# Optimization experiments

Hardware: AMD Instinct MI355X
Metric: run time of the kernel (lower is better)

Reference implementation:

```python
import jax, jax.numpy as jnp
import numpy as np

H = 2048      # hidden_dim
NH = 32       # num_heads
HD = H // NH  # head_dim


def setup_inputs() -> dict:
    key = jax.random.key(0)
    ks = jax.random.split(key, 9)
    s = 1.0 / np.sqrt(H)
    return {
        "hidden_states": jax.random.normal(ks[0], (2, 2048, H), dtype=jnp.float32),
        "wq": jax.random.uniform(ks[1], (H, H), jnp.float32, -s, s),
        "bq": jnp.zeros((H,), jnp.float32),
        "wk": jax.random.uniform(ks[2], (H, H), jnp.float32, -s, s),
        "bk": jnp.zeros((H,), jnp.float32),
        "wv": jax.random.uniform(ks[3], (H, H), jnp.float32, -s, s),
        "bv": jnp.zeros((H,), jnp.float32),
        "wo": jax.random.uniform(ks[4], (H, H), jnp.float32, -s, s),
        "bo": jnp.zeros((H,), jnp.float32),
    }


def reference(hidden_states, wq, bq, wk, bk, wv, bv, wo, bo):
    B, S, _ = hidden_states.shape
    def heads(x):  # [B,S,H] -> [B,NH,S,HD]
        return x.reshape(B, S, NH, HD).transpose(0, 2, 1, 3)
    q = heads(hidden_states @ wq.T + bq)
    k = heads(hidden_states @ wk.T + bk)
    v = heads(hidden_states @ wv.T + bv)
    scores = jnp.einsum("bhqd,bhkd->bhqk", q, k) / np.sqrt(HD).astype(np.float32)
    causal = jnp.tril(jnp.ones((S, S), dtype=bool))
    scores = jnp.where(causal, scores, -jnp.inf)
    attn = jax.nn.softmax(scores, axis=-1)
    out = jnp.einsum("bhqk,bhkd->bhqd", attn, v)
    out = out.transpose(0, 2, 1, 3).reshape(B, S, H)
    return out @ wo.T + bo
```

## Files before the change

### kernel.cpp

```cpp
#include <hip/hip_runtime.h>
#include <hip/hip_bf16.h>

#define HDIM 2048
#define NHEADS 32
#define HEADD 64
#define NBATCH 2
#define SEQLEN 2048
#define MTOT (NBATCH * SEQLEN)
#define NQT (SEQLEN / 128)
#define LDQKV 6144

typedef __bf16 bf16;
typedef __bf16 bf16x8 __attribute__((ext_vector_type(8)));
typedef float f32x4 __attribute__((ext_vector_type(4)));
typedef float f32x8 __attribute__((ext_vector_type(8)));
typedef float f32x16 __attribute__((ext_vector_type(16)));

__device__ __forceinline__ void gload_lds16(const bf16* g, bf16* l) {
  __builtin_amdgcn_global_load_lds(
      (const __attribute__((address_space(1))) void*)g,
      (__attribute__((address_space(3))) void*)l, 16, 0, 0);
}

__device__ __forceinline__ unsigned cvtpk_bf16(float lo, float hi) {
  unsigned r;
  asm("v_cvt_pk_bf16_f32 %0, %1, %2" : "=v"(r) : "v"(lo), "v"(hi));
  return r;
}

__device__ __forceinline__ float max3f(float a, float b, float c) {
  float r;
  asm("v_max3_f32 %0, %1, %2, %3" : "=v"(r) : "v"(a), "v"(b), "v"(c));
  return r;
}

__global__ void __launch_bounds__(256) cvt_f32_to_bf16(
    const float* __restrict__ src, bf16* __restrict__ dst, int n) {
  int i = (blockIdx.x * 256 + threadIdx.x) * 8;
  if (i >= n) return;
  f32x8 a = *(const f32x8*)(src + i);
  bf16x8 o;
#pragma unroll
  for (int j = 0; j < 8; ++j) o[j] = (bf16)a[j];
  *(bf16x8*)(dst + i) = o;
}

__global__ void __launch_bounds__(256) cvt4_f32_to_bf16(
    const float* __restrict__ s0, const float* __restrict__ s1,
    const float* __restrict__ s2, const float* __restrict__ s3,
    bf16* __restrict__ d0, bf16* __restrict__ d1,
    bf16* __restrict__ d2, bf16* __restrict__ d3) {
  const float* src; bf16* dst;
  switch (blockIdx.y) {
    case 0: src = s0; dst = d0; break;
    case 1: src = s1; dst = d1; break;
    case 2: src = s2; dst = d2; break;
    default: src = s3; dst = d3; break;
  }
  int i = (blockIdx.x * 256 + threadIdx.x) * 8;
  f32x8 a = *(const f32x8*)(src + i);
  bf16x8 o;
#pragma unroll
  for (int j = 0; j < 8; ++j) o[j] = (bf16)a[j];
  *(bf16x8*)(dst + i) = o;
}

__global__ void __launch_bounds__(256) pack_bias(
    const float* __restrict__ bq, const float* __restrict__ bk,
    const float* __restrict__ bv, float* __restrict__ out) {
  int i = blockIdx.x * 256 + threadIdx.x;
  if (i >= LDQKV) return;
  float v;
  if (i < HDIM) v = bq[i];
  else if (i < 2 * HDIM) v = bk[i - HDIM];
  else v = bv[i - 2 * HDIM];
  out[i] = v;
}

template <bool OUT_F32>
__global__ void __launch_bounds__(256, 2) gemmq(
    const bf16* __restrict__ A, const bf16* __restrict__ W,
    const float* __restrict__ bias, void* __restrict__ Cout,
    int Ndim, float scale) {
  constexpr int NT = 64;
  __shared__ bf16 As[2][256 * 32];
  __shared__ bf16 Bs[3][192 * 32];

  const int tid = threadIdx.x;
  const int l = tid & 63;
  const int w = tid >> 6;
  const int wm = w >> 1;
  const int wn = w & 1;

  const int wid = blockIdx.x;
  const int j = wid >> 3;
  const int m0 = ((wid & 7) * 2 + (j & 1)) * 256;
  const int n0 = (j >> 1) * 192;

  const int rowA = tid >> 2;
  const int cg = (((tid & 3) ^ ((tid >> 3) & 3))) * 8;

  auto stgA = [&](int s, int kt) {
    const bf16* g = A + (size_t)m0 * 2048 + kt * 32 + cg;
#pragma unroll
    for (int i = 0; i < 4; ++i)
      gload_lds16(g + (size_t)(i * 64 + rowA) * 2048,
                  &As[s][(i * 256 + w * 64) * 8]);
  };
  auto stgB = [&](int s, int kt) {
    const bf16* g = W + (size_t)n0 * 2048 + kt * 32 + cg;
#pragma unroll
    for (int i = 0; i < 3; ++i)
      gload_lds16(g + (size_t)(i * 64 + rowA) * 2048,
                  &Bs[s][(i * 256 + w * 64) * 8]);
  };

  f32x4 acc[8][6];
#pragma unroll
  for (int mf = 0; mf < 8; ++mf)
#pragma unroll
    for (int nf = 0; nf < 6; ++nf) acc[mf][nf] = {0.f, 0.f, 0.f, 0.f};

  const int fr = l & 15;
  const int fch = (((l >> 4) ^ ((fr >> 1) & 3))) * 8;
  const int abase = (wm * 128 + fr) * 32 + fch;
  const int bbase = (wn * 96 + fr) * 32 + fch;

  stgA(0, 0);
  stgB(0, 0);
  stgB(1, 1);
  asm volatile("s_waitcnt vmcnt(3)" ::: "memory");
  __builtin_amdgcn_s_barrier();

  int sb = 0;
  for (int t = 0; t < NT; ++t) {
    const int sa = t & 1;
    int sb2 = sb + 2; if (sb2 >= 3) sb2 -= 3;

    bf16x8 bf[6], af[4];
#pragma unroll
    for (int nf = 0; nf < 6; ++nf)
      bf[nf] = *(const bf16x8*)&Bs[sb][bbase + nf * 16 * 32];
#pragma unroll
    for (int f = 0; f < 4; ++f)
      af[f] = *(const bf16x8*)&As[sa][abase + f * 16 * 32];

    if (t + 1 < NT) stgA(sa ^ 1, t + 1);
    if (t + 2 < NT) stgB(sb2, t + 2);

    __builtin_amdgcn_s_setprio(1);
#pragma unroll
    for (int f = 0; f < 4; ++f)
#pragma unroll
      for (int nf = 0; nf < 6; ++nf)
        acc[f][nf] = __builtin_amdgcn_mfma_f32_16x16x32_bf16(
            af[f], bf[nf], acc[f][nf], 0, 0, 0);
    __builtin_amdgcn_s_setprio(0);

#pragma unroll
    for (int f = 0; f < 4; ++f)
      af[f] = *(const bf16x8*)&As[sa][abase + (4 + f) * 16 * 32];

    __builtin_amdgcn_s_setprio(1);
#pragma unroll
    for (int f = 0; f < 4; ++f)
#pragma unroll
      for (int nf = 0; nf < 6; ++nf)
        acc[4 + f][nf] = __builtin_amdgcn_mfma_f32_16x16x32_bf16(
            af[f], bf[nf], acc[4 + f][nf], 0, 0, 0);
    __builtin_amdgcn_s_setprio(0);

    if (t < NT - 2)
      asm volatile("s_waitcnt vmcnt(3)" ::: "memory");
    else
      asm volatile("s_waitcnt vmcnt(0)" ::: "memory");
    __builtin_amdgcn_s_barrier();

    sb = (sb == 2) ? 0 : sb + 1;
  }

  const int rj = (l >> 4) * 4;
#pragma unroll
  for (int mf = 0; mf < 8; ++mf)
#pragma unroll
    for (int nf = 0; nf < 6; ++nf) {
      const int col = n0 + wn * 96 + nf * 16 + fr;
      const float secsc = (col < 2048) ? scale : 1.0f;
      const float bvl = bias[col];
#pragma unroll
      for (int jj = 0; jj < 4; ++jj) {
        const int row = m0 + wm * 128 + mf * 16 + rj + jj;
        const float v = (acc[mf][nf][jj] + bvl) * secsc;
        if constexpr (OUT_F32)
          ((float*)Cout)[(size_t)row * Ndim + col] = v;
        else
          ((bf16*)Cout)[(size_t)row * Ndim + col] = (bf16)v;
      }
    }
}

template <int BM, bool OUT_F32>
__global__ void __launch_bounds__(512, 2) gemm3(
    const bf16* __restrict__ A, const bf16* __restrict__ W,
    const float* __restrict__ bias, void* __restrict__ Cout,
    int Ndim, float scale) {
  constexpr int NT = 64;
  constexpr int FM = BM / 32;
  constexpr int ALD = BM / 128;
  constexpr int LPT = ALD + 2;
  constexpr int MPX = (4096 / BM) / 8;
  __shared__ bf16 As[4][BM * 32];
  __shared__ bf16 Bs[4][256 * 32];

  const int tid = threadIdx.x;
  const int l = tid & 63;
  const int w = tid >> 6;
  const int wm = w >> 2;
  const int wn = w & 3;

  const int wid = blockIdx.x;
  const int j = wid >> 3;
  const int m0 = ((wid & 7) * MPX + (j & (MPX - 1))) * BM;
  const int n0 = (j / MPX) * 256;

  const float secsc = (n0 < 2048) ? scale : 1.0f;

  const int rowA = tid >> 2;
  const int cg = (((tid & 3) ^ ((tid >> 3) & 3))) * 8;

  auto stageA = [&](int s, int kt) {
    const int k0 = kt * 32 + cg;
#pragma unroll
    for (int i = 0; i < ALD; ++i)
      gload_lds16(A + (size_t)(m0 + i * 128 + rowA) * 2048 + k0,
                  &As[s][(i * 512 + w * 64) * 8]);
  };
  auto stageB = [&](int s, int kt) {
    const int k0 = kt * 32 + cg;
#pragma unroll
    for (int i = 0; i < 2; ++i)
      gload_lds16(W + (size_t)(n0 + i * 128 + rowA) * 2048 + k0,
                  &Bs[s][(i * 512 + w * 64) * 8]);
  };

  f32x4 acc[FM][4];
#pragma unroll
  for (int mf = 0; mf < FM; ++mf)
#pragma unroll
    for (int nf = 0; nf < 4; ++nf) acc[mf][nf] = {0.f, 0.f, 0.f, 0.f};

  const int fr = l & 15;
  const int fch = (((l >> 4) ^ ((fr >> 1) & 3))) * 8;

  stageA(0, 0); stageB(0, 0);
  stageA(1, 1); stageB(1, 1);
  stageA(2, 2); stageB(2, 2);
  if constexpr (LPT == 4)
    asm volatile("s_waitcnt vmcnt(8)" ::: "memory");
  else
    asm volatile("s_waitcnt vmcnt(6)" ::: "memory");
  __builtin_amdgcn_s_barrier();

  for (int t = 0; t < NT; ++t) {
    const int s = t & 3;
    const int sn = (t + 3) & 3;
    const bool st = (t + 3) < NT;

    bf16x8 bf[4], af[FM];
#pragma unroll
    for (int nf = 0; nf < 4; ++nf)
      bf[nf] = *(const bf16x8*)&Bs[s][(wn * 64 + nf * 16 + fr) * 32 + fch];
#pragma unroll
    for (int f = 0; f < FM; ++f)
      af[f] = *(const bf16x8*)&As[s][(wm * (BM / 2) + f * 16 + fr) * 32 + fch];

    if (st) { stageA(sn, t + 3); stageB(sn, t + 3); }

    __builtin_amdgcn_s_setprio(1);
#pragma unroll
    for (int f = 0; f < FM; ++f)
#pragma unroll
      for (int nf = 0; nf < 4; ++nf)
        acc[f][nf] = __builtin_amdgcn_mfma_f32_16x16x32_bf16(
            af[f], bf[nf], acc[f][nf], 0, 0, 0);
    __builtin_amdgcn_s_setprio(0);

    if (t < NT - 3) {
      if constexpr (LPT == 4)
        asm volatile("s_waitcnt vmcnt(8)" ::: "memory");
      else
        asm volatile("s_waitcnt vmcnt(6)" ::: "memory");
    } else if (t == NT - 3) {
      if constexpr (LPT == 4)
        asm volatile("s_waitcnt vmcnt(4)" ::: "memory");
      else
        asm volatile("s_waitcnt vmcnt(3)" ::: "memory");
    } else if (t == NT - 2) {
      asm volatile("s_waitcnt vmcnt(0)" ::: "memory");
    }
    if (t < NT - 1) __builtin_amdgcn_s_barrier();
  }

  const int rj = (l >> 4) * 4;
#pragma unroll
  for (int mf = 0; mf < FM; ++mf)
#pragma unroll
    for (int nf = 0; nf < 4; ++nf) {
      const int col = n0 + wn * 64 + nf * 16 + fr;
      const float bvl = bias[col];
#pragma unroll
      for (int jj = 0; jj < 4; ++jj) {
        const int row = m0 + wm * (BM / 2) + mf * 16 + rj + jj;
        const float v = (acc[mf][nf][jj] + bvl) * secsc;
        if constexpr (OUT_F32)
          ((float*)Cout)[(size_t)row * Ndim + col] = v;
        else
          ((bf16*)Cout)[(size_t)row * Ndim + col] = (bf16)v;
      }
    }
}

__global__ void __launch_bounds__(256) transpose_v(
    const bf16* __restrict__ QKV, bf16* __restrict__ Vt) {
  __shared__ bf16 T[64][72];
  const int t = threadIdx.x;
  const int s0 = blockIdx.x * 64;
  const int h = blockIdx.y, b = blockIdx.z;
  const size_t inb = (size_t)b * SEQLEN * LDQKV + 2 * HDIM + (size_t)h * HEADD;
#pragma unroll
  for (int i = 0; i < 2; ++i) {
    const int idx = t + i * 256;
    const int r = idx >> 3, c = (idx & 7) * 8;
    *(bf16x8*)&T[r][c] = *(const bf16x8*)&QKV[inb + (size_t)(s0 + r) * LDQKV + c];
  }
  __syncthreads();
  const size_t outb = (size_t)(b * NHEADS + h) * HEADD * SEQLEN + s0;
#pragma unroll
  for (int i = 0; i < 2; ++i) {
    const int idx = t + i * 256;
    const int d = idx >> 3, cs = (idx & 7) * 8;
    bf16x8 o;
#pragma unroll
    for (int j = 0; j < 8; ++j) o[j] = T[cs + j][d];
    *(bf16x8*)&Vt[outb + (size_t)d * SEQLEN + cs] = o;
  }
}

__global__ void __launch_bounds__(256) attn4(
    const bf16* __restrict__ QKV, const bf16* __restrict__ Vt,
    bf16* __restrict__ O) {
  __shared__ bf16 Kl[2][64 * 64];
  __shared__ bf16 Vl[2][64 * 64];

  const int tid = threadIdx.x;
  const int l = tid & 63;
  const int w = tid >> 6;
  const int lq = l & 31;
  const int g = l >> 5;
  const int h = blockIdx.y, b = blockIdx.z;
  const size_t baseQ = (size_t)b * SEQLEN * LDQKV + (size_t)h * HEADD;
  const size_t baseK = baseQ + HDIM;
  const size_t baseV = (size_t)(b * NHEADS + h) * HEADD * SEQLEN;
  const size_t baseO = (size_t)b * SEQLEN * HDIM + (size_t)h * HEADD;

  const int L0 = w * 128 + l;
  const int L1 = w * 128 + 64 + l;
  const int r0 = L0 >> 3, gc0 = ((L0 & 7) ^ (r0 & 7)) * 8;
  const int r1 = L1 >> 3, gc1 = ((L1 & 7) ^ (r1 & 7)) * 8;
  const int dst0 = (w * 128) * 8;
  const int dst1 = (w * 128 + 64) * 8;

  auto stage = [&](int bufi, int kt) {
    const int k0s = kt * 64;
    gload_lds16(QKV + baseK + (size_t)(k0s + r0) * LDQKV + gc0, &Kl[bufi][dst0]);
    gload_lds16(QKV + baseK + (size_t)(k0s + r1) * LDQKV + gc1, &Kl[bufi][dst1]);
    gload_lds16(Vt + baseV + (size_t)r0 * SEQLEN + k0s + gc0, &Vl[bufi][dst0]);
    gload_lds16(Vt + baseV + (size_t)r1 * SEQLEN + k0s + gc1, &Vl[bufi][dst1]);
  };

#pragma unroll
  for (int seg = 0; seg < 2; ++seg) {
    const int qt = seg ? blockIdx.x : (NQT - 1 - blockIdx.x);
    const int q0 = qt * 128;
    const int qw = q0 + w * 32;
    const int qa = qw + lq;

    bf16x8 qf[4];
#pragma unroll
    for (int ks = 0; ks < 4; ++ks)
      qf[ks] = *(const bf16x8*)&QKV[baseQ + (size_t)qa * LDQKV + ks * 16 + g * 8];

    f32x16 oacc0, oacc1;
#pragma unroll
    for (int r = 0; r < 16; ++r) { oacc0[r] = 0.f; oacc1[r] = 0.f; }
    float mrun = -__builtin_inff(), lrun = 0.f;

    const int nkt = q0 / 64 + 2;
    stage(0, 0);

    for (int kt = 0; kt < nkt; ++kt) {
      const int cur = kt & 1;
      const int k0 = kt * 64;
      if (kt + 1 < nkt) {
        stage(cur ^ 1, kt + 1);
        asm volatile("s_waitcnt vmcnt(4)" ::: "memory");
      } else {
        asm volatile("s_waitcnt vmcnt(0)" ::: "memory");
      }
      __builtin_amdgcn_s_barrier();

      if (k0 <= qw + 31) {
        f32x16 st0, st1;
#pragma unroll
        for (int r = 0; r < 16; ++r) { st0[r] = 0.f; st1[r] = 0.f; }
        __builtin_amdgcn_s_setprio(1);
#pragma unroll
        for (int ks = 0; ks < 4; ++ks) {
          const int cr = (((2 * ks + g) ^ (lq & 7))) * 8;
          bf16x8 kf0 = *(const bf16x8*)&Kl[cur][lq * 64 + cr];
          bf16x8 kf1 = *(const bf16x8*)&Kl[cur][(32 + lq) * 64 + cr];
          st0 = __builtin_amdgcn_mfma_f32_32x32x16_bf16(kf0, qf[ks], st0, 0, 0, 0);
          st1 = __builtin_amdgcn_mfma_f32_32x32x16_bf16(kf1, qf[ks], st1, 0, 0, 0);
        }
        __builtin_amdgcn_s_setprio(0);

        if (k0 + 63 > qw) {
#pragma unroll
          for (int r = 0; r < 16; ++r) {
            const int ro = (r & 3) + 8 * (r >> 2) + 4 * g;
            if (k0 + ro > qa) st0[r] = -__builtin_inff();
            if (k0 + 32 + ro > qa) st1[r] = -__builtin_inff();
          }
        }

        float mx[8];
#pragma unroll
        for (int r = 0; r < 8; ++r)
          mx[r] = fmaxf(max3f(st0[r], st0[r + 8], st1[r]), st1[r + 8]);
        const float ma = max3f(mx[0], mx[1], mx[2]);
        const float mb = max3f(mx[3], mx[4], mx[5]);
        const float mc = max3f(mx[6], mx[7], ma);
        const float mtree = fmaxf(mb, mc);
        const float pm = fmaxf(mtree, __shfl_xor(mtree, 32));

        const float mnew = fmaxf(mrun, pm);
        if (!__all(pm - mrun <= 11.0f)) {
          const float sc = __builtin_amdgcn_exp2f(mrun - mnew);
          lrun *= sc;
#pragma unroll
          for (int r = 0; r < 16; ++r) {
            const int ro = (r & 3) + 8 * (r >> 2) + 4 * g;
            const float scr = __shfl(sc, ro);
            oacc0[r] *= scr;
            oacc1[r] *= scr;
          }
          mrun = mnew;
        }

#pragma unroll
        for (int r = 0; r < 16; ++r) {
          st0[r] = __builtin_amdgcn_exp2f(st0[r] - mrun);
          st1[r] = __builtin_amdgcn_exp2f(st1[r] - mrun);
        }
        float sm[8];
#pragma unroll
        for (int r = 0; r < 8; ++r)
          sm[r] = (st0[r] + st0[r + 8]) + (st1[r] + st1[r + 8]);
#pragma unroll
        for (int s = 4; s > 0; s >>= 1)
#pragma unroll
          for (int r = 0; r < 4; ++r)
            if (r < s) sm[r] += sm[r + s];
        lrun += sm[0] + __shfl_xor(sm[0], 32);

        unsigned wd0[8], wd1[8];
#pragma unroll
        for (int i = 0; i < 8; ++i) {
          wd0[i] = cvtpk_bf16(st0[2 * i], st0[2 * i + 1]);
          wd1[i] = cvtpk_bf16(st1[2 * i], st1[2 * i + 1]);
        }
        bf16x8 paf[4];
#pragma unroll
        for (int kt2 = 0; kt2 < 2; ++kt2)
#pragma unroll
          for (int hf = 0; hf < 2; ++hf) {
            const unsigned* wsrc = kt2 ? wd1 : wd0;
            const unsigned a0 = wsrc[hf * 4 + 0], a1 = wsrc[hf * 4 + 1];
            const unsigned b0 = wsrc[hf * 4 + 2], b1 = wsrc[hf * 4 + 3];
            const unsigned sb0 = (unsigned)__shfl_xor((int)b0, 32);
            const unsigned sb1 = (unsigned)__shfl_xor((int)b1, 32);
            const unsigned sa0 = (unsigned)__shfl_xor((int)a0, 32);
            const unsigned sa1 = (unsigned)__shfl_xor((int)a1, 32);
            union { unsigned u[4]; bf16x8 v; } fu;
            fu.u[0] = g ? sb0 : a0;
            fu.u[1] = g ? sb1 : a1;
            fu.u[2] = g ? b0 : sa0;
            fu.u[3] = g ? b1 : sa1;
            paf[kt2 * 2 + hf] = fu.v;
          }

        __builtin_amdgcn_s_setprio(1);
#pragma unroll
        for (int s = 0; s < 4; ++s) {
          const int cr = (((2 * s + g) ^ (lq & 7))) * 8;
          bf16x8 vf0 = *(const bf16x8*)&Vl[cur][lq * 64 + cr];
          bf16x8 vf1 = *(const bf16x8*)&Vl[cur][(32 + lq) * 64 + cr];
          oacc0 = __builtin_amdgcn_mfma_f32_32x32x16_bf16(paf[s], vf0, oacc0, 0, 0, 0);
          oacc1 = __builtin_amdgcn_mfma_f32_32x32x16_bf16(paf[s], vf1, oacc1, 0, 0, 0);
        }
        __builtin_amdgcn_s_setprio(0);
      }
      __builtin_amdgcn_s_barrier();
    }

#pragma unroll
    for (int r = 0; r < 16; ++r) {
      const int ro = (r & 3) + 8 * (r >> 2) + 4 * g;
      const float lr = __shfl(lrun, ro);
      const float inv = 1.0f / lr;
      O[baseO + (size_t)(qw + ro) * HDIM + lq] = (bf16)(oacc0[r] * inv);
      O[baseO + (size_t)(qw + ro) * HDIM + 32 + lq] = (bf16)(oacc1[r] * inv);
    }
  }
}

extern "C" void kernel_launch(void* const* d_in, const int* in_sizes, int n_in,
                              void* d_out, int out_size, void* d_ws, size_t ws_size,
                              hipStream_t stream) {
  (void)in_sizes; (void)n_in; (void)out_size; (void)ws_size;
  const float* hs = (const float*)d_in[0];
  const float* wq = (const float*)d_in[1];
  const float* bq = (const float*)d_in[2];
  const float* wk = (const float*)d_in[3];
  const float* bk = (const float*)d_in[4];
  const float* wv = (const float*)d_in[5];
  const float* bv = (const float*)d_in[6];
  const float* wo = (const float*)d_in[7];
  const float* bo = (const float*)d_in[8];

  char* wsp = (char*)d_ws;
  bf16* hsb  = (bf16*)wsp; wsp += (size_t)MTOT * HDIM * sizeof(bf16);
  bf16* wqb  = (bf16*)wsp; wsp += (size_t)HDIM * HDIM * sizeof(bf16);
  bf16* wkb  = (bf16*)wsp; wsp += (size_t)HDIM * HDIM * sizeof(bf16);
  bf16* wvb  = (bf16*)wsp; wsp += (size_t)HDIM * HDIM * sizeof(bf16);
  bf16* wob  = (bf16*)wsp; wsp += (size_t)HDIM * HDIM * sizeof(bf16);
  bf16* QKVb = (bf16*)wsp; wsp += (size_t)MTOT * LDQKV * sizeof(bf16);
  float* biasqkv = (float*)wsp; wsp += (size_t)LDQKV * sizeof(float);
  bf16* aob = hsb;
  bf16* Vtb = wqb;

  const int nHS = MTOT * HDIM;
  const int nW = HDIM * HDIM;
  cvt_f32_to_bf16<<<nHS / 2048, 256, 0, stream>>>(hs, hsb, nHS);
  dim3 gc(nW / 2048, 4);
  cvt4_f32_to_bf16<<<gc, 256, 0, stream>>>(wq, wk, wv, wo, wqb, wkb, wvb, wob);
  pack_bias<<<LDQKV / 256, 256, 0, stream>>>(bq, bk, bv, biasqkv);

  gemmq<false><<<dim3(512), 256, 0, stream>>>(
      hsb, wqb, biasqkv, QKVb, LDQKV, 0.125f * 1.44269504f);

  dim3 gt(SEQLEN / 64, NHEADS, NBATCH);
  transpose_v<<<gt, 256, 0, stream>>>(QKVb, Vtb);

  dim3 ga(NQT / 2, NHEADS, NBATCH);
  attn4<<<ga, 256, 0, stream>>>(QKVb, Vtb, aob);

  gemm3<128, true><<<dim3(32 * (HDIM / 256)), 512, 0, stream>>>(
      aob, wob, bo, (float*)d_out, HDIM, 1.0f);
}
```

Before: 245.1 us.

## Replace output projection GEMM with 128x128-tile kernel and asymmetric A/B buffering

The output projection moves from a 128x256 tile GEMM (512 threads, 256 blocks, 4-stage ring) to a 128x128 tile kernel (256 threads, 512 blocks). The new kernel double-buffers A (prefetch distance 1) and triple-buffers B (prefetch distance 2), which cuts LDS use and aims to fit more blocks per CU and fill all CUs on the 4096x2048 output. In exchange, each tile reuses less data and the shorter prefetch distance for A may expose more global load latency.

Result: no change. 246.1 us (+0.4%).

```diff
diff --git a/kernel.cpp b/kernel.cpp
--- a/kernel.cpp
+++ b/kernel.cpp
@@ -199,123 +199,105 @@
     }
 }
 
-template <int BM, bool OUT_F32>
-__global__ void __launch_bounds__(512, 2) gemm3(
+__global__ void __launch_bounds__(256, 2) gemmp(
     const bf16* __restrict__ A, const bf16* __restrict__ W,
-    const float* __restrict__ bias, void* __restrict__ Cout,
-    int Ndim, float scale) {
+    const float* __restrict__ bias, float* __restrict__ Cout,
+    int Ndim) {
   constexpr int NT = 64;
-  constexpr int FM = BM / 32;
-  constexpr int ALD = BM / 128;
-  constexpr int LPT = ALD + 2;
-  constexpr int MPX = (4096 / BM) / 8;
-  __shared__ bf16 As[4][BM * 32];
-  __shared__ bf16 Bs[4][256 * 32];
+  __shared__ bf16 As[2][128 * 32];
+  __shared__ bf16 Bs[3][128 * 32];
 
   const int tid = threadIdx.x;
   const int l = tid & 63;
   const int w = tid >> 6;
-  const int wm = w >> 2;
-  const int wn = w & 3;
+  const int wm = w >> 1;
+  const int wn = w & 1;
 
   const int wid = blockIdx.x;
   const int j = wid >> 3;
-  const int m0 = ((wid & 7) * MPX + (j & (MPX - 1))) * BM;
-  const int n0 = (j / MPX) * 256;
-
-  const float secsc = (n0 < 2048) ? scale : 1.0f;
+  const int m0 = ((wid & 7) * 4 + (j & 3)) * 128;
+  const int n0 = (j >> 2) * 128;
 
   const int rowA = tid >> 2;
   const int cg = (((tid & 3) ^ ((tid >> 3) & 3))) * 8;
 
-  auto stageA = [&](int s, int kt) {
-    const int k0 = kt * 32 + cg;
-#pragma unroll
-    for (int i = 0; i < ALD; ++i)
-      gload_lds16(A + (size_t)(m0 + i * 128 + rowA) * 2048 + k0,
-                  &As[s][(i * 512 + w * 64) * 8]);
+  auto stgA = [&](int s, int kt) {
+    const bf16* g = A + (size_t)m0 * 2048 + kt * 32 + cg;
+#pragma unroll
+    for (int i = 0; i < 2; ++i)
+      gload_lds16(g + (size_t)(i * 64 + rowA) * 2048,
+                  &As[s][(i * 256 + w * 64) * 8]);
   };
-  auto stageB = [&](int s, int kt) {
-    const int k0 = kt * 32 + cg;
+  auto stgB = [&](int s, int kt) {
+    const bf16* g = W + (size_t)n0 * 2048 + kt * 32 + cg;
 #pragma unroll
     for (int i = 0; i < 2; ++i)
-      gload_lds16(W + (size_t)(n0 + i * 128 + rowA) * 2048 + k0,
-                  &Bs[s][(i * 512 + w * 64) * 8]);
+      gload_lds16(g + (size_t)(i * 64 + rowA) * 2048,
+                  &Bs[s][(i * 256 + w * 64) * 8]);
   };
 
-  f32x4 acc[FM][4];
-#pragma unroll
-  for (int mf = 0; mf < FM; ++mf)
+  f32x4 acc[4][4];
+#pragma unroll
+  for (int mf = 0; mf < 4; ++mf)
 #pragma unroll
     for (int nf = 0; nf < 4; ++nf) acc[mf][nf] = {0.f, 0.f, 0.f, 0.f};
 
   const int fr = l & 15;
   const int fch = (((l >> 4) ^ ((fr >> 1) & 3))) * 8;
-
-  stageA(0, 0); stageB(0, 0);
-  stageA(1, 1); stageB(1, 1);
-  stageA(2, 2); stageB(2, 2);
-  if constexpr (LPT == 4)
-    asm volatile("s_waitcnt vmcnt(8)" ::: "memory");
-  else
-    asm volatile("s_waitcnt vmcnt(6)" ::: "memory");
+  const int abase = (wm * 64 + fr) * 32 + fch;
+  const int bbase = (wn * 64 + fr) * 32 + fch;
+
+  stgA(0, 0);
+  stgB(0, 0);
+  stgB(1, 1);
+  asm volatile("s_waitcnt vmcnt(2)" ::: "memory");
   __builtin_amdgcn_s_barrier();
 
+  int sb = 0;
   for (int t = 0; t < NT; ++t) {
-    const int s = t & 3;
-    const int sn = (t + 3) & 3;
-    const bool st = (t + 3) < NT;
-
-    bf16x8 bf[4], af[FM];
+    const int sa = t & 1;
+    int sb2 = sb + 2; if (sb2 >= 3) sb2 -= 3;
+
+    bf16x8 bf[4], af[4];
 #pragma unroll
     for (int nf = 0; nf < 4; ++nf)
-      bf[nf] = *(const bf16x8*)&Bs[s][(wn * 64 + nf * 16 + fr) * 32 + fch];
-#pragma unroll
-    for (int f = 0; f < FM; ++f)
-      af[f] = *(const bf16x8*)&As[s][(wm * (BM / 2) + f * 16 + fr) * 32 + fch];
-
-    if (st) { stageA(sn, t + 3); stageB(sn, t + 3); }
+      bf[nf] = *(const bf16x8*)&Bs[sb][bbase + nf * 16 * 32];
+#pragma unroll
+    for (int f = 0; f < 4; ++f)
+      af[f] = *(const bf16x8*)&As[sa][abase + f * 16 * 32];
+
+    if (t + 1 < NT) stgA(sa ^ 1, t + 1);
+    if (t + 2 < NT) stgB(sb2, t + 2);
 
     __builtin_amdgcn_s_setprio(1);
 #pragma unroll
-    for (int f = 0; f < FM; ++f)
+    for (int f = 0; f < 4; ++f)
 #pragma unroll
       for (int nf = 0; nf < 4; ++nf)
         acc[f][nf] = __builtin_amdgcn_mfma_f32_16x16x32_bf16(
             af[f], bf[nf], acc[f][nf], 0, 0, 0);
     __builtin_amdgcn_s_setprio(0);
 
-    if (t < NT - 3) {
-      if constexpr (LPT == 4)
-        asm volatile("s_waitcnt vmcnt(8)" ::: "memory");
-      else
-        asm volatile("s_waitcnt vmcnt(6)" ::: "memory");
-    } else if (t == NT - 3) {
-      if constexpr (LPT == 4)
-        asm volatile("s_waitcnt vmcnt(4)" ::: "memory");
-      else
-        asm volatile("s_waitcnt vmcnt(3)" ::: "memory");
-    } else if (t == NT - 2) {
+    if (t < NT - 2)
+      asm volatile("s_waitcnt vmcnt(2)" ::: "memory");
+    else
       asm volatile("s_waitcnt vmcnt(0)" ::: "memory");
-    }
-    if (t < NT - 1) __builtin_amdgcn_s_barrier();
+    __builtin_amdgcn_s_barrier();
+
+    sb = (sb == 2) ? 0 : sb + 1;
   }
 
   const int rj = (l >> 4) * 4;
 #pragma unroll
-  for (int mf = 0; mf < FM; ++mf)
+  for (int mf = 0; mf < 4; ++mf)
 #pragma unroll
     for (int nf = 0; nf < 4; ++nf) {
       const int col = n0 + wn * 64 + nf * 16 + fr;
       const float bvl = bias[col];
 #pragma unroll
       for (int jj = 0; jj < 4; ++jj) {
-        const int row = m0 + wm * (BM / 2) + mf * 16 + rj + jj;
-        const float v = (acc[mf][nf][jj] + bvl) * secsc;
-        if constexpr (OUT_F32)
-          ((float*)Cout)[(size_t)row * Ndim + col] = v;
-        else
-          ((bf16*)Cout)[(size_t)row * Ndim + col] = (bf16)v;
+        const int row = m0 + wm * 64 + mf * 16 + rj + jj;
+        Cout[(size_t)row * Ndim + col] = acc[mf][nf][jj] + bvl;
       }
     }
 }
@@ -565,6 +547,5 @@
   dim3 ga(NQT / 2, NHEADS, NBATCH);
   attn4<<<ga, 256, 0, stream>>>(QKVb, Vtb, aob);
 
-  gemm3<128, true><<<dim3(32 * (HDIM / 256)), 512, 0, stream>>>(
-      aob, wob, bo, (float*)d_out, HDIM, 1.0f);
-}
+  gemmp<<<dim3(512), 256, 0, stream>>>(aob, wob, bo, (float*)d_out, HDIM);
+}
```
